# Kernel tuning notes

Measured on AMD Instinct MI355X. Metric: run time of the kernel, lower is better.

## Reference

```python
import jax, jax.numpy as jnp
import numpy as np

B, HW, DIM, HEADS, HEAD_DIM, MLP_DIM, WS = 64, 56, 384, 12, 32, 1536, 7
INNER = HEADS * HEAD_DIM
NEG = -1e9


def _masks():
    ws, d = WS, WS // 2
    ul = np.zeros((ws * ws, ws * ws), np.float32)
    ul[-d * ws:, :-d * ws] = NEG
    ul[:-d * ws, -d * ws:] = NEG
    lr = np.zeros((ws, ws, ws, ws), np.float32)
    lr[:, -d:, :, :-d] = NEG
    lr[:, :-d, :, -d:] = NEG
    return jnp.asarray(ul), jnp.asarray(lr.reshape(ws * ws, ws * ws))


def _rel_indices():
    # pairwise relative 2D offsets between the ws*ws positions in a window
    idx = np.stack(np.meshgrid(np.arange(WS), np.arange(WS), indexing='ij'), -1).reshape(-1, 2)
    rel = idx[None, :, :] - idx[:, None, :] + (WS - 1)  # values in [0, 2*WS-2]
    return jnp.asarray(rel)


def _ln(x, g, b):
    m = x.mean(-1, keepdims=True)
    v = x.var(-1, keepdims=True)
    return (x - m) * jax.lax.rsqrt(v + 1e-5) * g + b


def _window_attention(x, w_qkv, pos_emb, w_out, b_out):
    b = x.shape[0]
    disp = WS // 2
    nw = HW // WS  # windows per side
    x = jnp.roll(x, (-disp, -disp), axis=(1, 2))  # cyclic shift
    qkv = x @ w_qkv  # [b, H, W, 3*inner]
    q, k, v = jnp.split(qkv, 3, axis=-1)

    def part(t):  # b (nw w1) (nw w2) (h d) -> b h (nw*nw) (w1*w2) d
        t = t.reshape(b, nw, WS, nw, WS, HEADS, HEAD_DIM)
        return t.transpose(0, 5, 1, 3, 2, 4, 6).reshape(b, HEADS, nw * nw, WS * WS, HEAD_DIM)

    q, k, v = part(q), part(k), part(v)
    dots = jnp.einsum('bhwid,bhwjd->bhwij', q, k) * (HEAD_DIM ** -0.5)
    rel = _rel_indices()
    dots = dots + pos_emb[rel[..., 0], rel[..., 1]]  # relative position bias
    ul, lr = _masks()
    dots = dots.at[:, :, -nw:].add(ul)            # bottom row of windows
    dots = dots.at[:, :, nw - 1::nw].add(lr)      # rightmost column of windows
    attn = jax.nn.softmax(dots, axis=-1)
    out = jnp.einsum('bhwij,bhwjd->bhwid', attn, v)
    # b h (nw nw) (w1 w2) d -> b (nw w1) (nw w2) (h d)
    out = out.reshape(b, HEADS, nw, nw, WS, WS, HEAD_DIM)
    out = out.transpose(0, 2, 4, 3, 5, 1, 6).reshape(b, HW, HW, INNER)
    out = out @ w_out + b_out
    return jnp.roll(out, (disp, disp), axis=(1, 2))  # cyclic back-shift


def swin_block(x, w_qkv, pos_emb, w_out, b_out, ln1_g, ln1_b, ln2_g, ln2_b,
               w_mlp1, b_mlp1, w_mlp2, b_mlp2):
    x = x + _window_attention(_ln(x, ln1_g, ln1_b), w_qkv, pos_emb, w_out, b_out)
    h = _ln(x, ln2_g, ln2_b)
    h = jax.nn.gelu(h @ w_mlp1 + b_mlp1) @ w_mlp2 + b_mlp2
    return x + h


def setup_inputs() -> dict:
    key = jax.random.key(0)
    ks = jax.random.split(key, 8)
    s = lambda fan_in: fan_in ** -0.5
    return {
        'x': jax.random.normal(ks[0], (B, HW, HW, DIM), jnp.float32),
        'w_qkv': jax.random.normal(ks[1], (DIM, 3 * INNER), jnp.float32) * s(DIM),
        'pos_emb': jax.random.normal(ks[2], (2 * WS - 1, 2 * WS - 1), jnp.float32),
        'w_out': jax.random.normal(ks[3], (INNER, DIM), jnp.float32) * s(INNER),
        'b_out': jnp.zeros((DIM,), jnp.float32),
        'ln1_g': jnp.ones((DIM,), jnp.float32),
        'ln1_b': jnp.zeros((DIM,), jnp.float32),
        'ln2_g': jnp.ones((DIM,), jnp.float32),
        'ln2_b': jnp.zeros((DIM,), jnp.float32),
        'w_mlp1': jax.random.normal(ks[4], (DIM, MLP_DIM), jnp.float32) * s(DIM),
        'b_mlp1': jnp.zeros((MLP_DIM,), jnp.float32),
        'w_mlp2': jax.random.normal(ks[5], (MLP_DIM, DIM), jnp.float32) * s(MLP_DIM),
        'b_mlp2': jnp.zeros((DIM,), jnp.float32),
    }


def reference(x, w_qkv, pos_emb, w_out, b_out, ln1_g, ln1_b, ln2_g, ln2_b,
              w_mlp1, b_mlp1, w_mlp2, b_mlp2):
    return swin_block(x, w_qkv, pos_emb, w_out, b_out, ln1_g, ln1_b, ln2_g, ln2_b,
                      w_mlp1, b_mlp1, w_mlp2, b_mlp2)
```

## Files before the change

### kernel.cpp

```cpp
#include <hip/hip_runtime.h>
#include <stdint.h>
#include <stddef.h>


typedef unsigned short u16;
typedef __attribute__((ext_vector_type(8))) short bf16x8;
typedef __attribute__((ext_vector_type(8))) unsigned short u16x8;
typedef __attribute__((ext_vector_type(4))) float f32x4;
typedef __attribute__((ext_vector_type(2))) float f32x2;

#define HW2 3136

__device__ __forceinline__ u16 f2bf(float f) {
    unsigned u = __float_as_uint(f);
    return (u16)((u + 0x7FFFu + ((u >> 16) & 1u)) >> 16);
}

__device__ __forceinline__ f32x4 mfma16(bf16x8 a, bf16x8 b, f32x4 c) {
    return __builtin_amdgcn_mfma_f32_16x16x32_bf16(a, b, c, 0, 0, 0);
}

__device__ __forceinline__ void a_copy16(const void* g, void* l) {
    __builtin_amdgcn_global_load_lds((const __attribute__((address_space(1))) void*)g,
                                     (__attribute__((address_space(3))) void*)l, 16, 0, 0);
}

__global__ __launch_bounds__(256) void wtrans(const float* __restrict__ w,
                                              u16* __restrict__ wt, int K, int N) {
    long tid = (long)blockIdx.x * 256 + threadIdx.x;
    if (tid >= (long)K * N) return;
    int n = (int)(tid / K), k = (int)(tid % K);
    wt[tid] = f2bf(w[(long)k * N + n]);
}

__global__ __launch_bounds__(256) void prep_tab(const float* __restrict__ pe,
                                                float* __restrict__ tab) {
    int tid = blockIdx.x * 256 + threadIdx.x;
    if (tid >= 4 * 2401) return;
    int cb = tid / 2401, rem = tid % 2401;
    int i = rem / 49, j = rem % 49;
    int ix = i % 7, jx = j % 7;
    int iy = i / 7, jy = j / 7;
    float v = pe[(jy - iy + 6) * 13 + (jx - ix + 6)];
    if ((cb & 1) && ((i >= 28) != (j >= 28))) v += -1e9f;
    if ((cb & 2) && ((ix >= 4) != (jx >= 4))) v += -1e9f;
    tab[tid] = v;
}

template <int SHIFT>
__global__ __launch_bounds__(256) void ln_kernel(const float* __restrict__ in,
                                                 u16* __restrict__ out,
                                                 const float* __restrict__ gw,
                                                 const float* __restrict__ bw) {
    const int lane = threadIdx.x & 63;
    const int wave = threadIdx.x >> 6;
    const long t = (long)blockIdx.x * 4 + wave;
    const float* row = in + t * 384;
    f32x2 v0 = *(const f32x2*)(row + lane * 2);
    f32x2 v1 = *(const f32x2*)(row + 128 + lane * 2);
    f32x2 v2 = *(const f32x2*)(row + 256 + lane * 2);
    float s = v0.x + v0.y + v1.x + v1.y + v2.x + v2.y;
    float q = v0.x * v0.x + v0.y * v0.y + v1.x * v1.x + v1.y * v1.y + v2.x * v2.x + v2.y * v2.y;
#pragma unroll
    for (int m = 1; m < 64; m <<= 1) {
        s += __shfl_xor(s, m);
        q += __shfl_xor(q, m);
    }
    const float mean = s * (1.f / 384.f);
    const float rstd = rsqrtf(q * (1.f / 384.f) - mean * mean + 1e-5f);
    long orow = t;
    if (SHIFT) {
        long b = t / HW2;
        int rem = (int)(t % HW2);
        int y = rem / 56 - 3; if (y < 0) y += 56;
        int x = rem % 56 - 3; if (x < 0) x += 56;
        orow = b * HW2 + y * 56 + x;
    }
    u16* po = out + orow * 384;
#pragma unroll
    for (int p = 0; p < 3; p++) {
        f32x2 vv = (p == 0) ? v0 : ((p == 1) ? v1 : v2);
        f32x2 gg = *(const f32x2*)(gw + p * 128 + lane * 2);
        f32x2 bb = *(const f32x2*)(bw + p * 128 + lane * 2);
        float a0 = (vv.x - mean) * rstd * gg.x + bb.x;
        float a1 = (vv.y - mean) * rstd * gg.y + bb.y;
        unsigned pk = (unsigned)f2bf(a0) | ((unsigned)f2bf(a1) << 16);
        *(unsigned*)(po + p * 128 + lane * 2) = pk;
    }
}

template <int EPI>
__global__ __launch_bounds__(256, 4) void gemm_bf16(const u16* __restrict__ A,
                                                    const u16* __restrict__ Bt,
                                                    int N, int K,
                                                    const float* __restrict__ bias,
                                                    const float* resid,
                                                    float* outf, u16* outb) {
    __shared__ u16 Abuf[8192];
    __shared__ u16 Bbuf[8192];
    int bid = blockIdx.x;
    if ((gridDim.x & 7) == 0) {
        const int cpx = gridDim.x >> 3;
        bid = (bid & 7) * cpx + (bid >> 3);
    }
    const int ntiles = N >> 7;
    const long m0 = (long)(bid / ntiles) << 7;
    const int n0 = (bid % ntiles) << 7;
    const int lane = threadIdx.x & 63;
    const int wave = threadIdx.x >> 6;
    const int wr = (wave >> 1) << 6;
    const int wc = (wave & 1) << 6;
    const int lr = lane & 15;
    const int g  = lane >> 4;

    const u16* aP0; const u16* aP1; const u16* aP2; const u16* aP3;
    const u16* bP0; const u16* bP1; const u16* bP2; const u16* bP3;
    int d0, d1, d2, d3;
    {
#define STAGE_INIT(j, aP, bP, dd)                                          \
        {                                                                  \
            const int o = (((j << 2) + wave) << 10) + lane * 16;           \
            const int row = o >> 7;                                        \
            const int slot = (o >> 4) & 7;                                 \
            const int ce = ((slot ^ (row & 7)) << 3);                      \
            aP = A + (size_t)(m0 + row) * K + ce;                          \
            bP = Bt + (size_t)(n0 + row) * K + ce;                         \
            dd = o >> 1;                                                   \
        }
        STAGE_INIT(0, aP0, bP0, d0)
        STAGE_INIT(1, aP1, bP1, d1)
        STAGE_INIT(2, aP2, bP2, d2)
        STAGE_INIT(3, aP3, bP3, d3)
#undef STAGE_INIT
    }

    f32x4 acc[4][4];
#pragma unroll
    for (int i = 0; i < 4; i++)
#pragma unroll
        for (int j = 0; j < 4; j++) acc[i][j] = (f32x4){0.f, 0.f, 0.f, 0.f};

    for (int k0 = 0; k0 < K; k0 += 64) {
        __syncthreads();
        a_copy16(aP0, Abuf + d0); a_copy16(bP0, Bbuf + d0); aP0 += 64; bP0 += 64;
        a_copy16(aP1, Abuf + d1); a_copy16(bP1, Bbuf + d1); aP1 += 64; bP1 += 64;
        a_copy16(aP2, Abuf + d2); a_copy16(bP2, Bbuf + d2); aP2 += 64; bP2 += 64;
        a_copy16(aP3, Abuf + d3); a_copy16(bP3, Bbuf + d3); aP3 += 64; bP3 += 64;
        __syncthreads();
#pragma unroll
        for (int t = 0; t < 2; t++) {
            bf16x8 bfr[4];
#pragma unroll
            for (int ni = 0; ni < 4; ni++) {
                const int row = wc + ni * 16 + lr;
                const int slot = ((t << 2) + g) ^ (row & 7);
                bfr[ni] = *(const bf16x8*)(Bbuf + row * 64 + slot * 8);
            }
#pragma unroll
            for (int mi = 0; mi < 4; mi++) {
                const int row = wr + mi * 16 + lr;
                const int slot = ((t << 2) + g) ^ (row & 7);
                const bf16x8 af = *(const bf16x8*)(Abuf + row * 64 + slot * 8);
#pragma unroll
                for (int ni = 0; ni < 4; ni++)
                    acc[mi][ni] = mfma16(af, bfr[ni], acc[mi][ni]);
            }
        }
    }

    const int g4 = g << 2;
    float bs[4];
    if (EPI != 0) {
#pragma unroll
        for (int ni = 0; ni < 4; ni++) bs[ni] = bias[n0 + wc + ni * 16 + lr];
    }
#pragma unroll
    for (int mi = 0; mi < 4; mi++) {
#pragma unroll
        for (int r = 0; r < 4; r++) {
            const long m = m0 + wr + mi * 16 + g4 + r;
            long mo = m;
            if (EPI == 1) {
                long b = m / HW2;
                int rem = (int)(m % HW2);
                int y = rem / 56 + 3; if (y >= 56) y -= 56;
                int x = rem % 56 + 3; if (x >= 56) x -= 56;
                mo = b * HW2 + y * 56 + x;
            }
            u16* pb = (EPI == 0 || EPI == 2) ? outb + (size_t)m * N + n0 + wc + lr : nullptr;
            float* pf = (EPI == 1 || EPI == 3) ? outf + (size_t)mo * 384 + n0 + wc + lr : nullptr;
            const float* pr = (EPI == 1 || EPI == 3)
                                  ? resid + (size_t)mo * 384 + n0 + wc + lr : nullptr;
#pragma unroll
            for (int ni = 0; ni < 4; ni++) {
                const float v = acc[mi][ni][r];
                if (EPI == 0) {
                    pb[ni * 16] = f2bf(v);
                } else if (EPI == 1 || EPI == 3) {
                    pf[ni * 16] = pr[ni * 16] + v + bs[ni];
                } else {
                    const float gx = v + bs[ni];
                    const float y = 0.7978845608028654f * gx * (1.f + 0.044715f * gx * gx);
                    const float e = __expf(-2.f * y);
                    pb[ni * 16] = f2bf(gx * __builtin_amdgcn_rcpf(1.f + e));
                }
            }
        }
    }
}

__global__ __launch_bounds__(256) void attn_kernel(const u16* __restrict__ qkv,
                                                   const float* __restrict__ tab,
                                                   u16* __restrict__ outa) {
    __shared__ u16 sVt[4][2304];
    __shared__ u16 sP[4][4608];
    const int lane = threadIdx.x & 63;
    const int wave = threadIdx.x >> 6;
    const int bid = blockIdx.x;
    const int hg = bid % 3;
    const int win = (bid / 3) & 63;
    const int b = bid / 192;
    const int wy = win >> 3, wx = win & 7;
    const int head = hg * 4 + wave;
    const long wbase = (long)b * HW2 + (long)wy * 392 + wx * 7;
    const int c = lane & 15, g = lane >> 4;
    const int kk = g << 3;

    u16* vt = sVt[wave];
    for (int i = lane; i < 2304; i += 64) vt[i] = 0;
    if (lane < 49) {
        const long mr = wbase + (lane / 7) * 56 + (lane % 7);
        const u16* vr = qkv + mr * 1152 + 768 + head * 32;
#pragma unroll
        for (int u = 0; u < 4; u++) {
            u16x8 vv = *(const u16x8*)(vr + u * 8);
#pragma unroll
            for (int e = 0; e < 8; e++) vt[(u * 8 + e) * 72 + lane] = vv[e];
        }
    }

    bf16x8 aq[4], bk[4];
#pragma unroll
    for (int mi = 0; mi < 4; mi++) {
        int t = mi * 16 + c; t = t > 48 ? 48 : t;
        const long mr = wbase + (t / 7) * 56 + (t % 7);
        aq[mi] = *(const bf16x8*)(qkv + mr * 1152 + head * 32 + kk);
    }
#pragma unroll
    for (int ni = 0; ni < 4; ni++) {
        int t = ni * 16 + c; t = t > 48 ? 48 : t;
        const long mr = wbase + (t / 7) * 56 + (t % 7);
        bk[ni] = *(const bf16x8*)(qkv + mr * 1152 + 384 + head * 32 + kk);
    }

    f32x4 sc[4][4];
#pragma unroll
    for (int i = 0; i < 4; i++)
#pragma unroll
        for (int j = 0; j < 4; j++) sc[i][j] = (f32x4){0.f, 0.f, 0.f, 0.f};
#pragma unroll
    for (int mi = 0; mi < 4; mi++)
#pragma unroll
        for (int ni = 0; ni < 4; ni++) sc[mi][ni] = mfma16(aq[mi], bk[ni], sc[mi][ni]);

    const float* tb = tab + (((wy == 7) ? 1 : 0) | ((wx == 7) ? 2 : 0)) * 2401;
#pragma unroll
    for (int mi = 0; mi < 4; mi++) {
#pragma unroll
        for (int r = 0; r < 4; r++) {
            int i = mi * 16 + (g << 2) + r;
            int ic = i > 48 ? 48 : i;
#pragma unroll
            for (int ni = 0; ni < 4; ni++) {
                int j = ni * 16 + c;
                float sv;
                if (j < 49)
                    sv = sc[mi][ni][r] * 0.17677669529663689f + tb[ic * 49 + j];
                else
                    sv = -3.0e38f;
                sc[mi][ni][r] = sv;
            }
        }
    }

    u16* pp = sP[wave];
#pragma unroll
    for (int mi = 0; mi < 4; mi++) {
#pragma unroll
        for (int r = 0; r < 4; r++) {
            float sm = fmaxf(fmaxf(sc[mi][0][r], sc[mi][1][r]),
                             fmaxf(sc[mi][2][r], sc[mi][3][r]));
            sm = fmaxf(sm, __shfl_xor(sm, 1));
            sm = fmaxf(sm, __shfl_xor(sm, 2));
            sm = fmaxf(sm, __shfl_xor(sm, 4));
            sm = fmaxf(sm, __shfl_xor(sm, 8));
            float p0 = __expf(sc[mi][0][r] - sm);
            float p1 = __expf(sc[mi][1][r] - sm);
            float p2 = __expf(sc[mi][2][r] - sm);
            float p3 = __expf(sc[mi][3][r] - sm);
            float ss = p0 + p1 + p2 + p3;
            ss += __shfl_xor(ss, 1);
            ss += __shfl_xor(ss, 2);
            ss += __shfl_xor(ss, 4);
            ss += __shfl_xor(ss, 8);
            const float ri = 1.f / ss;
            const int i = mi * 16 + (g << 2) + r;
            pp[i * 72 + c] = f2bf(p0 * ri);
            pp[i * 72 + 16 + c] = f2bf(p1 * ri);
            pp[i * 72 + 32 + c] = f2bf(p2 * ri);
            pp[i * 72 + 48 + c] = f2bf(p3 * ri);
        }
    }
    __syncthreads();

    f32x4 oc[4][2];
#pragma unroll
    for (int i = 0; i < 4; i++) {
        oc[i][0] = (f32x4){0.f, 0.f, 0.f, 0.f};
        oc[i][1] = (f32x4){0.f, 0.f, 0.f, 0.f};
    }
#pragma unroll
    for (int ks = 0; ks < 2; ks++) {
        bf16x8 bv0 = *(const bf16x8*)(vt + c * 72 + kk + ks * 32);
        bf16x8 bv1 = *(const bf16x8*)(vt + (16 + c) * 72 + kk + ks * 32);
#pragma unroll
        for (int mi = 0; mi < 4; mi++) {
            bf16x8 ap = *(const bf16x8*)(pp + (mi * 16 + c) * 72 + kk + ks * 32);
            oc[mi][0] = mfma16(ap, bv0, oc[mi][0]);
            oc[mi][1] = mfma16(ap, bv1, oc[mi][1]);
        }
    }

#pragma unroll
    for (int mi = 0; mi < 4; mi++) {
#pragma unroll
        for (int r = 0; r < 4; r++) {
            const int i = mi * 16 + (g << 2) + r;
            if (i < 49) {
                const long mr = wbase + (i / 7) * 56 + (i % 7);
                u16* po = outa + mr * 384 + head * 32;
                po[c] = f2bf(oc[mi][0][r]);
                po[16 + c] = f2bf(oc[mi][1][r]);
            }
        }
    }
}

extern "C" void kernel_launch(void* const* d_in, const int* in_sizes, int n_in,
                              void* d_out, int out_size, void* d_ws, size_t ws_size,
                              hipStream_t stream) {
    (void)in_sizes; (void)n_in; (void)out_size;
    const float* x     = (const float*)d_in[0];
    const float* w_qkv = (const float*)d_in[1];
    const float* pos   = (const float*)d_in[2];
    const float* w_out = (const float*)d_in[3];
    const float* b_out = (const float*)d_in[4];
    const float* ln1g  = (const float*)d_in[5];
    const float* ln1b  = (const float*)d_in[6];
    const float* ln2g  = (const float*)d_in[7];
    const float* ln2b  = (const float*)d_in[8];
    const float* w1    = (const float*)d_in[9];
    const float* b1    = (const float*)d_in[10];
    const float* w2    = (const float*)d_in[11];
    const float* b2    = (const float*)d_in[12];
    float* out = (float*)d_out;
    char* ws = (char*)d_ws;

    u16* wqkvT  = (u16*)(ws + 0);
    u16* woutT  = (u16*)(ws + 884736);
    u16* wm1T   = (u16*)(ws + 1179648);
    u16* wm2T   = (u16*)(ws + 2359296);
    float* tab  = (float*)(ws + 3538944);
    const size_t pool0 = 3577856;
    const size_t avail = (ws_size > pool0) ? ws_size - pool0 : 0;

    int CH = 64;
    while (CH > 2 && (size_t)CH * 12042240ULL > avail) CH >>= 1;
    const int nchunks = 64 / CH;
    u16* bufA = (u16*)(ws + pool0);
    u16* bufB = (u16*)(ws + pool0 + (size_t)CH * 2408448ULL);
    const int rows = CH * HW2;
    const int tiles = rows >> 7;

    wtrans<<<1728, 256, 0, stream>>>(w_qkv, wqkvT, 384, 1152);
    wtrans<<<576, 256, 0, stream>>>(w_out, woutT, 384, 384);
    wtrans<<<2304, 256, 0, stream>>>(w1, wm1T, 384, 1536);
    wtrans<<<2304, 256, 0, stream>>>(w2, wm2T, 1536, 384);
    prep_tab<<<38, 256, 0, stream>>>(pos, tab);

    for (int c = 0; c < nchunks; ++c) {
        const float* xc = x + (size_t)c * rows * 384;
        float* oc = out + (size_t)c * rows * 384;
        u16* attc = bufB + (size_t)rows * 1152;
        ln_kernel<1><<<rows / 4, 256, 0, stream>>>(xc, bufA, ln1g, ln1b);
        gemm_bf16<0><<<tiles * 9, 256, 0, stream>>>(bufA, wqkvT, 1152, 384,
                                                    nullptr, nullptr, nullptr, bufB);
        attn_kernel<<<CH * 192, 256, 0, stream>>>(bufB, tab, attc);
        gemm_bf16<1><<<tiles * 3, 256, 0, stream>>>(attc, woutT, 384, 384,
                                                    b_out, xc, oc, nullptr);
    }

    for (int c = 0; c < nchunks; ++c) {
        float* xr = out + (size_t)c * rows * 384;
        ln_kernel<0><<<rows / 4, 256, 0, stream>>>(xr, bufA, ln2g, ln2b);
        gemm_bf16<2><<<tiles * 12, 256, 0, stream>>>(bufA, wm1T, 1536, 384,
                                                     b1, nullptr, nullptr, bufB);
        gemm_bf16<3><<<tiles * 3, 256, 0, stream>>>(bufB, wm2T, 384, 1536,
                                                    b2, xr, xr, nullptr);
    }
}
```

Baseline: 1.887 ms.

## Keep attention residual in bf16 and fuse MLP into per-chunk loop

The attention output plus residual is now stored as a bf16 intermediate in workspace instead of fp32 in the output buffer. LN2 and the final MLP residual read that bf16 copy, and the MLP stage runs inside the same chunk loop as attention. Chunk size is capped at 16 batches so the intermediates stay smaller and likelier to hit cache. This cuts fp32 traffic for the intermediate residual, but rounding the residual stream to bf16 adds precision loss, and a smaller chunk means more kernel launches.

```diff
diff --git a/kernel.cpp b/kernel.cpp
--- a/kernel.cpp
+++ b/kernel.cpp
@@ -16,6 +16,10 @@
     return (u16)((u + 0x7FFFu + ((u >> 16) & 1u)) >> 16);
 }
 
+__device__ __forceinline__ float bf2f(u16 u) {
+    return __uint_as_float((unsigned)u << 16);
+}
+
 __device__ __forceinline__ f32x4 mfma16(bf16x8 a, bf16x8 b, f32x4 c) {
     return __builtin_amdgcn_mfma_f32_16x16x32_bf16(a, b, c, 0, 0, 0);
 }
@@ -23,6 +27,15 @@
 __device__ __forceinline__ void a_copy16(const void* g, void* l) {
     __builtin_amdgcn_global_load_lds((const __attribute__((address_space(1))) void*)g,
                                      (__attribute__((address_space(3))) void*)l, 16, 0, 0);
+}
+
+__device__ __forceinline__ f32x2 ld2(const float* p) { return *(const f32x2*)p; }
+__device__ __forceinline__ f32x2 ld2(const u16* p) {
+    const unsigned u = *(const unsigned*)p;
+    f32x2 r;
+    r.x = __uint_as_float(u << 16);
+    r.y = __uint_as_float(u & 0xffff0000u);
+    return r;
 }
 
 __global__ __launch_bounds__(256) void wtrans(const float* __restrict__ w,
@@ -47,18 +60,18 @@
     tab[tid] = v;
 }
 
-template <int SHIFT>
-__global__ __launch_bounds__(256) void ln_kernel(const float* __restrict__ in,
+template <int SHIFT, typename TIN>
+__global__ __launch_bounds__(256) void ln_kernel(const TIN* __restrict__ in,
                                                  u16* __restrict__ out,
                                                  const float* __restrict__ gw,
                                                  const float* __restrict__ bw) {
     const int lane = threadIdx.x & 63;
     const int wave = threadIdx.x >> 6;
     const long t = (long)blockIdx.x * 4 + wave;
-    const float* row = in + t * 384;
-    f32x2 v0 = *(const f32x2*)(row + lane * 2);
-    f32x2 v1 = *(const f32x2*)(row + 128 + lane * 2);
-    f32x2 v2 = *(const f32x2*)(row + 256 + lane * 2);
+    const TIN* row = in + t * 384;
+    f32x2 v0 = ld2(row + lane * 2);
+    f32x2 v1 = ld2(row + 128 + lane * 2);
+    f32x2 v2 = ld2(row + 256 + lane * 2);
     float s = v0.x + v0.y + v1.x + v1.y + v2.x + v2.y;
     float q = v0.x * v0.x + v0.y * v0.y + v1.x * v1.x + v1.y * v1.y + v2.x * v2.x + v2.y * v2.y;
 #pragma unroll
@@ -94,7 +107,7 @@
                                                     const u16* __restrict__ Bt,
                                                     int N, int K,
                                                     const float* __restrict__ bias,
-                                                    const float* resid,
+                                                    const void* residv,
                                                     float* outf, u16* outb) {
     __shared__ u16 Abuf[8192];
     __shared__ u16 Bbuf[8192];
@@ -168,6 +181,8 @@
         }
     }
 
+    const float* residf = (const float*)residv;
+    const u16*  residb  = (const u16*)residv;
     const int g4 = g << 2;
     float bs[4];
     if (EPI != 0) {
@@ -187,22 +202,23 @@
                 int x = rem % 56 + 3; if (x >= 56) x -= 56;
                 mo = b * HW2 + y * 56 + x;
             }
-            u16* pb = (EPI == 0 || EPI == 2) ? outb + (size_t)m * N + n0 + wc + lr : nullptr;
-            float* pf = (EPI == 1 || EPI == 3) ? outf + (size_t)mo * 384 + n0 + wc + lr : nullptr;
-            const float* pr = (EPI == 1 || EPI == 3)
-                                  ? resid + (size_t)mo * 384 + n0 + wc + lr : nullptr;
 #pragma unroll
             for (int ni = 0; ni < 4; ni++) {
                 const float v = acc[mi][ni][r];
+                const int n = n0 + wc + ni * 16 + lr;
                 if (EPI == 0) {
-                    pb[ni * 16] = f2bf(v);
-                } else if (EPI == 1 || EPI == 3) {
-                    pf[ni * 16] = pr[ni * 16] + v + bs[ni];
-                } else {
+                    outb[(size_t)m * N + n] = f2bf(v);
+                } else if (EPI == 1) {
+                    const size_t o = (size_t)mo * 384 + n;
+                    outb[o] = f2bf(residf[o] + v + bs[ni]);
+                } else if (EPI == 2) {
                     const float gx = v + bs[ni];
                     const float y = 0.7978845608028654f * gx * (1.f + 0.044715f * gx * gx);
                     const float e = __expf(-2.f * y);
-                    pb[ni * 16] = f2bf(gx * __builtin_amdgcn_rcpf(1.f + e));
+                    outb[(size_t)m * N + n] = f2bf(gx * __builtin_amdgcn_rcpf(1.f + e));
+                } else {
+                    const size_t o = (size_t)m * 384 + n;
+                    outf[o] = bf2f(residb[o]) + v + bs[ni];
                 }
             }
         }
@@ -374,13 +390,15 @@
     const size_t pool0 = 3577856;
     const size_t avail = (ws_size > pool0) ? ws_size - pool0 : 0;
 
-    int CH = 64;
-    while (CH > 2 && (size_t)CH * 12042240ULL > avail) CH >>= 1;
+    int CH = 16;
+    while (CH > 2 && (size_t)CH * 3136 * 4608ULL > avail) CH >>= 1;
     const int nchunks = 64 / CH;
-    u16* bufA = (u16*)(ws + pool0);
-    u16* bufB = (u16*)(ws + pool0 + (size_t)CH * 2408448ULL);
     const int rows = CH * HW2;
     const int tiles = rows >> 7;
+    u16* bufA = (u16*)(ws + pool0);
+    u16* bufB = bufA + (size_t)rows * 384;
+    u16* bufC = bufB + (size_t)rows * 1152;
+    u16* bufD = bufC + (size_t)rows * 384;
 
     wtrans<<<1728, 256, 0, stream>>>(w_qkv, wqkvT, 384, 1152);
     wtrans<<<576, 256, 0, stream>>>(w_out, woutT, 384, 384);
@@ -391,21 +409,16 @@
     for (int c = 0; c < nchunks; ++c) {
         const float* xc = x + (size_t)c * rows * 384;
         float* oc = out + (size_t)c * rows * 384;
-        u16* attc = bufB + (size_t)rows * 1152;
-        ln_kernel<1><<<rows / 4, 256, 0, stream>>>(xc, bufA, ln1g, ln1b);
+        ln_kernel<1, float><<<rows / 4, 256, 0, stream>>>(xc, bufA, ln1g, ln1b);
         gemm_bf16<0><<<tiles * 9, 256, 0, stream>>>(bufA, wqkvT, 1152, 384,
                                                     nullptr, nullptr, nullptr, bufB);
-        attn_kernel<<<CH * 192, 256, 0, stream>>>(bufB, tab, attc);
-        gemm_bf16<1><<<tiles * 3, 256, 0, stream>>>(attc, woutT, 384, 384,
-                                                    b_out, xc, oc, nullptr);
-    }
-
-    for (int c = 0; c < nchunks; ++c) {
-        float* xr = out + (size_t)c * rows * 384;
-        ln_kernel<0><<<rows / 4, 256, 0, stream>>>(xr, bufA, ln2g, ln2b);
+        attn_kernel<<<CH * 192, 256, 0, stream>>>(bufB, tab, bufC);
+        gemm_bf16<1><<<tiles * 3, 256, 0, stream>>>(bufC, woutT, 384, 384,
+                                                    b_out, xc, nullptr, bufD);
+        ln_kernel<0, u16><<<rows / 4, 256, 0, stream>>>(bufD, bufA, ln2g, ln2b);
         gemm_bf16<2><<<tiles * 12, 256, 0, stream>>>(bufA, wm1T, 1536, 384,
                                                      b1, nullptr, nullptr, bufB);
         gemm_bf16<3><<<tiles * 3, 256, 0, stream>>>(bufB, wm2T, 384, 1536,
-                                                    b2, xr, xr, nullptr);
-    }
-}
+                                                    b2, bufD, oc, nullptr);
+    }
+}
```

Measured after the change: 1.569 ms. 1.2x faster.
